# Performance work log

Hardware: AMD Instinct MI355X
Metric: run time of the kernel (lower is better)

## Reference

```python
import jax, jax.numpy as jnp
import numpy as np

B, N, NE, C = 1, 50000, 400000, 128
NTOK, NHEAD = 64, 4
HID = 256


def setup_inputs() -> dict:
    key = jax.random.key(0)
    ks = jax.random.split(key, 48)
    i = [0]
    def nx(shape, s=0.05):
        k = ks[i[0]]; i[0] += 1
        return jax.random.normal(k, shape, jnp.float32) * s
    inp = {}
    inp['V'] = nx((B, N, C), 1.0)
    inp['E'] = nx((B, NE, C), 1.0)
    kidx = ks[i[0]]; i[0] += 1
    inp['edges'] = jax.random.randint(kidx, (B, NE, 2), 0, N, dtype=jnp.int32)
    inp['F_space'] = jnp.zeros((B, N, 45), jnp.float32)
    # GNN f_edge: Linear(384->256), GELU, Linear(256->128), LayerNorm(128)
    inp['fe_w1'] = nx((HID, 3 * C)); inp['fe_b1'] = nx((HID,))
    inp['fe_w2'] = nx((C, HID));     inp['fe_b2'] = nx((C,))
    inp['fe_g'] = jnp.ones((C,));    inp['fe_be'] = jnp.zeros((C,))
    # GNN f_node: Linear(256->256), GELU, Linear(256->128), LayerNorm(128)
    inp['fn_w1'] = nx((HID, 2 * C)); inp['fn_b1'] = nx((HID,))
    inp['fn_w2'] = nx((C, HID));     inp['fn_b2'] = nx((C,))
    inp['fn_g'] = jnp.ones((C,));    inp['fn_be'] = jnp.zeros((C,))
    inp['ln1_g'] = jnp.ones((C,));   inp['ln1_b'] = jnp.zeros((C,))
    inp['ln2_g'] = jnp.ones((C,));   inp['ln2_b'] = jnp.zeros((C,))
    inp['lin_w'] = nx((C, C));       inp['lin_b'] = nx((C,))
    # AttentionBlock params
    inp['Qp'] = nx((NTOK, C), 1.0)
    inp['q1_w'] = nx((C, C)); inp['q1_b'] = nx((C,))
    inp['k1_w'] = nx((C, C)); inp['k1_b'] = nx((C,))
    inp['v1_w'] = nx((C, C)); inp['v1_b'] = nx((C,))
    inp['mha_in_w'] = nx((3 * C, C)); inp['mha_in_b'] = nx((3 * C,))
    inp['mha_out_w'] = nx((C, C));    inp['mha_out_b'] = nx((C,))
    inp['q2_w'] = nx((C, C)); inp['q2_b'] = nx((C,))
    inp['k2_w'] = nx((C, C)); inp['k2_b'] = nx((C,))
    inp['v2_w'] = nx((C, C)); inp['v2_b'] = nx((C,))
    # alphas (init 0 in the original; randomized here so gates are non-trivial)
    inp['a1'] = nx((1,), 0.5); inp['a2'] = nx((1,), 0.5)
    inp['a3'] = nx((1,), 0.5); inp['a4'] = nx((1,), 0.5)
    return inp


def _ln(x, g, b, eps=1e-5):
    m = jnp.mean(x, -1, keepdims=True)
    v = jnp.mean((x - m) ** 2, -1, keepdims=True)
    return (x - m) / jnp.sqrt(v + eps) * g + b


def _lin(x, w, b):
    return x @ w.T + b


def _gelu(x):
    return jax.nn.gelu(x, approximate=False)


def reference(V, E, edges, F_space, fe_w1, fe_b1, fe_w2, fe_b2, fe_g, fe_be,
              fn_w1, fn_b1, fn_w2, fn_b2, fn_g, fn_be, ln1_g, ln1_b, ln2_g, ln2_b,
              lin_w, lin_b, Qp, q1_w, q1_b, k1_w, k1_b, v1_w, v1_b,
              mha_in_w, mha_in_b, mha_out_w, mha_out_b, q2_w, q2_b, k2_w, k2_b,
              v2_w, v2_b, a1, a2, a3, a4):
    b, n, c = V.shape
    ne = edges.shape[1]
    # ---- GNN: gather -> edge MLP -> scatter_mean -> node MLP ----
    senders = jnp.take_along_axis(V, edges[..., 0:1], axis=1)    # [B,Ne,C]
    receivers = jnp.take_along_axis(V, edges[..., 1:2], axis=1)  # [B,Ne,C]
    edge_inpt = jnp.concatenate([senders, receivers, E], axis=-1)  # [B,Ne,3C]
    e_emb = _ln(_lin(_gelu(_lin(edge_inpt, fe_w1, fe_b1)), fe_w2, fe_b2), fe_g, fe_be)
    seg = (edges[..., 1] + jnp.arange(b, dtype=edges.dtype)[:, None] * n).reshape(-1)
    esum = jax.ops.segment_sum(e_emb.reshape(b * ne, c), seg, num_segments=b * n)
    cnt = jax.ops.segment_sum(jnp.ones((b * ne,), e_emb.dtype), seg, num_segments=b * n)
    edge_mean = (esum / jnp.maximum(cnt, 1.0)[:, None]).reshape(b, n, c)
    node_inpt = jnp.concatenate([V, edge_mean], axis=-1)
    v_emb = _ln(_lin(_gelu(_lin(node_inpt, fn_w1, fn_b1)), fn_w2, fn_b2), fn_g, fn_be)
    # ---- gated residuals (idx=0 < n_blocks=4) ----
    silu = jax.nn.silu
    Vr = V + silu(a1) * v_emb
    E_out = E + silu(a2) * e_emb
    # ---- dual cross-attention ----
    W0 = _ln(Vr, ln1_g, ln1_b)
    scale = c ** (-0.5)
    Q1 = _lin(jnp.broadcast_to(Qp, (b, NTOK, c)), q1_w, q1_b)
    K1 = _lin(W0, k1_w, k1_b)
    V1 = _lin(W0, v1_w, v1_b)
    attn1 = jax.nn.softmax(jnp.einsum('bmc,bnc->bmn', Q1, K1) * scale, axis=-1)
    W1 = attn1 @ V1  # [B,NTOK,C]
    # nn.MultiheadAttention(W1, W1, W1)
    h = c // NHEAD
    qkv = W1 @ mha_in_w.T + mha_in_b
    q, k, v = jnp.split(qkv, 3, axis=-1)
    sp = lambda t: t.reshape(b, NTOK, NHEAD, h).transpose(0, 2, 1, 3)
    q, k, v = sp(q), sp(k), sp(v)
    a = jax.nn.softmax(jnp.einsum('bhqd,bhkd->bhqk', q, k) * (h ** -0.5), axis=-1)
    o = jnp.einsum('bhqk,bhkd->bhqd', a, v).transpose(0, 2, 1, 3).reshape(b, NTOK, c)
    W2 = o @ mha_out_w.T + mha_out_b
    Q2 = _lin(W0, q2_w, q2_b)
    K2 = _lin(W2, k2_w, k2_b)
    V2 = _lin(W2, v2_w, v2_b)
    attn2 = jax.nn.softmax(jnp.einsum('bnc,bmc->bnm', Q2, K2) * scale, axis=-1)
    W3a = attn2 @ V2  # [B,N,C]
    W2r = Vr + silu(a3) * W3a
    W3 = W2r + silu(a4) * _lin(_ln(W2r, ln2_g, ln2_b), lin_w, lin_b)
    return (W3, E_out)
```

## Files before the change

### kernel.cpp

```cpp
#include <hip/hip_runtime.h>
#include <hip/hip_bf16.h>

#define NN 50000
#define NEDGE 400000
#define CDIM 128
#define NSP 50048

typedef short bf16x8 __attribute__((ext_vector_type(8)));
typedef short bf16x4 __attribute__((ext_vector_type(4)));
typedef float f32x4 __attribute__((ext_vector_type(4)));

__device__ __forceinline__ short f2b(float f) {
  union { float f; unsigned u; } a; a.f = f;
  unsigned u = a.u;
  u += 0x7fffu + ((u >> 16) & 1u);
  return (short)(u >> 16);
}
__device__ __forceinline__ float b2f(short s) {
  union { unsigned u; float f; } a; a.u = ((unsigned)(unsigned short)s) << 16;
  return a.f;
}
__device__ __forceinline__ float geluf(float x) {
  return 0.5f * x * (1.0f + erff(x * 0.7071067811865475f));
}
__device__ __forceinline__ f32x4 mfma16(bf16x8 a, bf16x8 b, f32x4 c) {
  return __builtin_amdgcn_mfma_f32_16x16x32_bf16(a, b, c, 0, 0, 0);
}

__global__ __launch_bounds__(256) void prep_kernel(
    const float* few1, const float* few2, const float* fnw1, const float* fnw2,
    const float* k1w, const float* v1w, const float* q2w,
    const float* k1b, const float* v1b, const float* q2b,
    const float* linw,
    short* wb1, short* wb2, short* wn1, short* wn2,
    short* wkvq, float* bkvq, short* wlin)
{
  int i = blockIdx.x * blockDim.x + threadIdx.x;
  int nthr = gridDim.x * blockDim.x;
  const float scale = 0.0883883476483184f;
  for (int idx = i; idx < 98304; idx += nthr) wb1[idx] = f2b(few1[idx]);
  for (int idx = i; idx < 32768; idx += nthr) wb2[idx] = f2b(few2[idx]);
  for (int idx = i; idx < 65536; idx += nthr) wn1[idx] = f2b(fnw1[idx]);
  for (int idx = i; idx < 32768; idx += nthr) wn2[idx] = f2b(fnw2[idx]);
  for (int idx = i; idx < 16384; idx += nthr) {
    wkvq[idx]         = f2b(k1w[idx]);
    wkvq[16384 + idx] = f2b(v1w[idx]);
    wkvq[32768 + idx] = f2b(q2w[idx] * scale);
    wlin[idx]         = f2b(linw[idx]);
  }
  for (int idx = i; idx < 128; idx += nthr) {
    bkvq[idx]       = k1b[idx];
    bkvq[128 + idx] = v1b[idx];
    bkvq[256 + idx] = q2b[idx] * scale;
  }
}

__global__ __launch_bounds__(256) void q1_kernel(
    const float* Qp, const float* q1w, const float* q1b, short* q1bf)
{
  int idx = blockIdx.x * 256 + threadIdx.x;
  int m = idx >> 7, n = idx & 127;
  const float scale = 0.0883883476483184f;
  float s = q1b[n];
  const float* qr = Qp + m * CDIM;
  const float* wr = q1w + n * CDIM;
  for (int k = 0; k < CDIM; k++) s += qr[k] * wr[k];
  q1bf[idx] = f2b(s * scale);
}

__global__ __launch_bounds__(256) void edge_kernel(
    const float* __restrict__ V, const float* __restrict__ E,
    const int* __restrict__ edges,
    const short* __restrict__ wb1, const float* __restrict__ fb1,
    const short* __restrict__ wb2, const float* __restrict__ fb2,
    const float* __restrict__ feg, const float* __restrict__ febe,
    const float* __restrict__ a2p,
    float* __restrict__ accn, float* __restrict__ cnt,
    float* __restrict__ outE)
{
  __shared__ short xs[64 * 392];
  __shared__ float redS[64][4], redQ[64][4];
  __shared__ int recvl[64];
  const int t = threadIdx.x;
  const int e0 = blockIdx.x * 64;
  if (t < 64) recvl[t] = edges[(e0 + t) * 2 + 1];
#pragma unroll
  for (int p = 0; p < 24; p++) {
    int fid = p * 256 + t;
    int row = fid / 96;
    int c = fid - row * 96;
    int seg = c >> 5;
    int c4 = c & 31;
    const float* src;
    if (seg == 0)      src = V + (size_t)edges[(e0 + row) * 2]     * CDIM + c4 * 4;
    else if (seg == 1) src = V + (size_t)edges[(e0 + row) * 2 + 1] * CDIM + c4 * 4;
    else               src = E + (size_t)(e0 + row) * CDIM + c4 * 4;
    f32x4 v = *(const f32x4*)src;
    bf16x4 bb; bb[0] = f2b(v[0]); bb[1] = f2b(v[1]); bb[2] = f2b(v[2]); bb[3] = f2b(v[3]);
    *(bf16x4*)(&xs[row * 392 + seg * 128 + c4 * 4]) = bb;
  }
  __syncthreads();
  const int lane = t & 63, wid = t >> 6;
  const int lr = lane & 15;
  const int g4 = (lane >> 4) * 4;
  const int lk = (lane >> 4) * 8;
  f32x4 acc1[4][4];
#pragma unroll
  for (int nt = 0; nt < 4; nt++) {
    float bv = fb1[wid * 64 + nt * 16 + lr];
#pragma unroll
    for (int mt = 0; mt < 4; mt++) acc1[mt][nt] = (f32x4){bv, bv, bv, bv};
  }
  for (int s = 0; s < 12; s++) {
    bf16x8 af[4];
#pragma unroll
    for (int mt = 0; mt < 4; mt++)
      af[mt] = *(const bf16x8*)(&xs[(mt * 16 + lr) * 392 + s * 32 + lk]);
#pragma unroll
    for (int nt = 0; nt < 4; nt++) {
      bf16x8 bf = *(const bf16x8*)(wb1 + (size_t)(wid * 64 + nt * 16 + lr) * 384 + s * 32 + lk);
#pragma unroll
      for (int mt = 0; mt < 4; mt++) acc1[mt][nt] = mfma16(af[mt], bf, acc1[mt][nt]);
    }
  }
  __syncthreads();
  short* hs = xs;
#pragma unroll
  for (int mt = 0; mt < 4; mt++)
#pragma unroll
    for (int nt = 0; nt < 4; nt++)
#pragma unroll
      for (int i = 0; i < 4; i++)
        hs[(mt * 16 + g4 + i) * 264 + wid * 64 + nt * 16 + lr] = f2b(geluf(acc1[mt][nt][i]));
  __syncthreads();
  f32x4 acc2[4][2];
#pragma unroll
  for (int nt = 0; nt < 2; nt++) {
    float bv = fb2[wid * 32 + nt * 16 + lr];
#pragma unroll
    for (int mt = 0; mt < 4; mt++) acc2[mt][nt] = (f32x4){bv, bv, bv, bv};
  }
  for (int s = 0; s < 8; s++) {
    bf16x8 af[4];
#pragma unroll
    for (int mt = 0; mt < 4; mt++)
      af[mt] = *(const bf16x8*)(&hs[(mt * 16 + lr) * 264 + s * 32 + lk]);
#pragma unroll
    for (int nt = 0; nt < 2; nt++) {
      bf16x8 bf = *(const bf16x8*)(wb2 + (size_t)(wid * 32 + nt * 16 + lr) * 256 + s * 32 + lk);
#pragma unroll
      for (int mt = 0; mt < 4; mt++) acc2[mt][nt] = mfma16(af[mt], bf, acc2[mt][nt]);
    }
  }
#pragma unroll
  for (int mt = 0; mt < 4; mt++)
#pragma unroll
    for (int i = 0; i < 4; i++) {
      float s1 = acc2[mt][0][i] + acc2[mt][1][i];
      float s2 = acc2[mt][0][i] * acc2[mt][0][i] + acc2[mt][1][i] * acc2[mt][1][i];
#pragma unroll
      for (int m = 1; m <= 8; m <<= 1) { s1 += __shfl_xor(s1, m); s2 += __shfl_xor(s2, m); }
      if (lr == 0) { redS[mt * 16 + g4 + i][wid] = s1; redQ[mt * 16 + g4 + i][wid] = s2; }
    }
  __syncthreads();
  float a2v = a2p[0];
  float sa2 = a2v / (1.0f + __expf(-a2v));
  float mean[4][4], rstd[4][4];
#pragma unroll
  for (int mt = 0; mt < 4; mt++)
#pragma unroll
    for (int i = 0; i < 4; i++) {
      int row = mt * 16 + g4 + i;
      float s1 = redS[row][0] + redS[row][1] + redS[row][2] + redS[row][3];
      float s2 = redQ[row][0] + redQ[row][1] + redQ[row][2] + redQ[row][3];
      float mn = s1 * (1.0f / 128.0f);
      float var = s2 * (1.0f / 128.0f) - mn * mn;
      mean[mt][i] = mn;
      rstd[mt][i] = rsqrtf(var + 1e-5f);
    }
#pragma unroll
  for (int nt = 0; nt < 2; nt++) {
    int col = wid * 32 + nt * 16 + lr;
    float gg = feg[col], bb = febe[col];
#pragma unroll
    for (int mt = 0; mt < 4; mt++)
#pragma unroll
      for (int i = 0; i < 4; i++) {
        int row = mt * 16 + g4 + i;
        float v = (acc2[mt][nt][i] - mean[mt][i]) * rstd[mt][i] * gg + bb;
        size_t ge = (size_t)(e0 + row) * CDIM + col;
        outE[ge] = E[ge] + sa2 * v;
        atomicAdd(&accn[(size_t)recvl[row] * CDIM + col], v);
      }
  }
  if (wid == 0 && lr == 0) {
#pragma unroll
    for (int mt = 0; mt < 4; mt++)
#pragma unroll
      for (int i = 0; i < 4; i++)
        atomicAdd(&cnt[recvl[mt * 16 + g4 + i]], 1.0f);
  }
}

__global__ __launch_bounds__(256) void node_kernel(
    const float* __restrict__ V, const float* __restrict__ accn, const float* __restrict__ cnt,
    const short* __restrict__ wn1, const float* __restrict__ fnb1,
    const short* __restrict__ wn2, const float* __restrict__ fnb2,
    const float* __restrict__ fng, const float* __restrict__ fnbe,
    const float* __restrict__ ln1g, const float* __restrict__ ln1b,
    const float* __restrict__ a1p,
    float* __restrict__ Vr, short* __restrict__ W0bf)
{
  __shared__ short xs[64 * 264];
  __shared__ float redS[64][4], redQ[64][4], redS2[64][4], redQ2[64][4];
  const int t = threadIdx.x;
  const int n0 = blockIdx.x * 64;
#pragma unroll
  for (int p = 0; p < 16; p++) {
    int fid = p * 256 + t;
    int row = fid >> 6;
    int c = fid & 63;
    int node = n0 + row; if (node >= NN) node = NN - 1;
    f32x4 v;
    if (c < 32) v = *(const f32x4*)(V + (size_t)node * CDIM + c * 4);
    else {
      v = *(const f32x4*)(accn + (size_t)node * CDIM + (c - 32) * 4);
      float ic = 1.0f / fmaxf(cnt[node], 1.0f);
      v[0] *= ic; v[1] *= ic; v[2] *= ic; v[3] *= ic;
    }
    bf16x4 bb; bb[0] = f2b(v[0]); bb[1] = f2b(v[1]); bb[2] = f2b(v[2]); bb[3] = f2b(v[3]);
    *(bf16x4*)(&xs[row * 264 + c * 4]) = bb;
  }
  __syncthreads();
  const int lane = t & 63, wid = t >> 6;
  const int lr = lane & 15;
  const int g4 = (lane >> 4) * 4;
  const int lk = (lane >> 4) * 8;
  f32x4 acc1[4][4];
#pragma unroll
  for (int nt = 0; nt < 4; nt++) {
    float bv = fnb1[wid * 64 + nt * 16 + lr];
#pragma unroll
    for (int mt = 0; mt < 4; mt++) acc1[mt][nt] = (f32x4){bv, bv, bv, bv};
  }
  for (int s = 0; s < 8; s++) {
    bf16x8 af[4];
#pragma unroll
    for (int mt = 0; mt < 4; mt++)
      af[mt] = *(const bf16x8*)(&xs[(mt * 16 + lr) * 264 + s * 32 + lk]);
#pragma unroll
    for (int nt = 0; nt < 4; nt++) {
      bf16x8 bf = *(const bf16x8*)(wn1 + (size_t)(wid * 64 + nt * 16 + lr) * 256 + s * 32 + lk);
#pragma unroll
      for (int mt = 0; mt < 4; mt++) acc1[mt][nt] = mfma16(af[mt], bf, acc1[mt][nt]);
    }
  }
  __syncthreads();
  short* hs = xs;
#pragma unroll
  for (int mt = 0; mt < 4; mt++)
#pragma unroll
    for (int nt = 0; nt < 4; nt++)
#pragma unroll
      for (int i = 0; i < 4; i++)
        hs[(mt * 16 + g4 + i) * 264 + wid * 64 + nt * 16 + lr] = f2b(geluf(acc1[mt][nt][i]));
  __syncthreads();
  f32x4 acc2[4][2];
#pragma unroll
  for (int nt = 0; nt < 2; nt++) {
    float bv = fnb2[wid * 32 + nt * 16 + lr];
#pragma unroll
    for (int mt = 0; mt < 4; mt++) acc2[mt][nt] = (f32x4){bv, bv, bv, bv};
  }
  for (int s = 0; s < 8; s++) {
    bf16x8 af[4];
#pragma unroll
    for (int mt = 0; mt < 4; mt++)
      af[mt] = *(const bf16x8*)(&hs[(mt * 16 + lr) * 264 + s * 32 + lk]);
#pragma unroll
    for (int nt = 0; nt < 2; nt++) {
      bf16x8 bf = *(const bf16x8*)(wn2 + (size_t)(wid * 32 + nt * 16 + lr) * 256 + s * 32 + lk);
#pragma unroll
      for (int mt = 0; mt < 4; mt++) acc2[mt][nt] = mfma16(af[mt], bf, acc2[mt][nt]);
    }
  }
#pragma unroll
  for (int mt = 0; mt < 4; mt++)
#pragma unroll
    for (int i = 0; i < 4; i++) {
      float s1 = acc2[mt][0][i] + acc2[mt][1][i];
      float s2 = acc2[mt][0][i] * acc2[mt][0][i] + acc2[mt][1][i] * acc2[mt][1][i];
#pragma unroll
      for (int m = 1; m <= 8; m <<= 1) { s1 += __shfl_xor(s1, m); s2 += __shfl_xor(s2, m); }
      if (lr == 0) { redS[mt * 16 + g4 + i][wid] = s1; redQ[mt * 16 + g4 + i][wid] = s2; }
    }
  __syncthreads();
  float a1v = a1p[0];
  float sa1 = a1v / (1.0f + __expf(-a1v));
  float mean[4][4], rstd[4][4];
#pragma unroll
  for (int mt = 0; mt < 4; mt++)
#pragma unroll
    for (int i = 0; i < 4; i++) {
      int row = mt * 16 + g4 + i;
      float s1 = redS[row][0] + redS[row][1] + redS[row][2] + redS[row][3];
      float s2 = redQ[row][0] + redQ[row][1] + redQ[row][2] + redQ[row][3];
      float mn = s1 * (1.0f / 128.0f);
      float var = s2 * (1.0f / 128.0f) - mn * mn;
      mean[mt][i] = mn; rstd[mt][i] = rsqrtf(var + 1e-5f);
    }
#pragma unroll
  for (int nt = 0; nt < 2; nt++) {
    int col = wid * 32 + nt * 16 + lr;
    float gg = fng[col], bb = fnbe[col];
#pragma unroll
    for (int mt = 0; mt < 4; mt++)
#pragma unroll
      for (int i = 0; i < 4; i++) {
        int row = mt * 16 + g4 + i;
        int node = n0 + row;
        int nc = node < NN ? node : NN - 1;
        float vemb = (acc2[mt][nt][i] - mean[mt][i]) * rstd[mt][i] * gg + bb;
        float vr = V[(size_t)nc * CDIM + col] + sa1 * vemb;
        acc2[mt][nt][i] = vr;
        if (node < NN) Vr[(size_t)node * CDIM + col] = vr;
      }
  }
#pragma unroll
  for (int mt = 0; mt < 4; mt++)
#pragma unroll
    for (int i = 0; i < 4; i++) {
      float s1 = acc2[mt][0][i] + acc2[mt][1][i];
      float s2 = acc2[mt][0][i] * acc2[mt][0][i] + acc2[mt][1][i] * acc2[mt][1][i];
#pragma unroll
      for (int m = 1; m <= 8; m <<= 1) { s1 += __shfl_xor(s1, m); s2 += __shfl_xor(s2, m); }
      if (lr == 0) { redS2[mt * 16 + g4 + i][wid] = s1; redQ2[mt * 16 + g4 + i][wid] = s2; }
    }
  __syncthreads();
#pragma unroll
  for (int mt = 0; mt < 4; mt++)
#pragma unroll
    for (int i = 0; i < 4; i++) {
      int row = mt * 16 + g4 + i;
      float s1 = redS2[row][0] + redS2[row][1] + redS2[row][2] + redS2[row][3];
      float s2 = redQ2[row][0] + redQ2[row][1] + redQ2[row][2] + redQ2[row][3];
      float mn = s1 * (1.0f / 128.0f);
      float var = s2 * (1.0f / 128.0f) - mn * mn;
      mean[mt][i] = mn; rstd[mt][i] = rsqrtf(var + 1e-5f);
    }
#pragma unroll
  for (int nt = 0; nt < 2; nt++) {
    int col = wid * 32 + nt * 16 + lr;
    float gg = ln1g[col], bb = ln1b[col];
#pragma unroll
    for (int mt = 0; mt < 4; mt++)
#pragma unroll
      for (int i = 0; i < 4; i++) {
        int row = mt * 16 + g4 + i;
        int node = n0 + row;
        if (node < NN)
          W0bf[(size_t)node * CDIM + col] =
              f2b((acc2[mt][nt][i] - mean[mt][i]) * rstd[mt][i] * gg + bb);
      }
  }
}

__global__ __launch_bounds__(256) void kvq_kernel(
    const short* __restrict__ W0bf, const short* __restrict__ wkvq,
    const float* __restrict__ bkvq,
    short* __restrict__ K1bf, short* __restrict__ V1bf, short* __restrict__ Q2bf)
{
  const int t = threadIdx.x, lane = t & 63, wid = t >> 6;
  const int n0 = blockIdx.x * 64;
  const int m0 = wid * 16, lr = lane & 15, lk = (lane >> 4) * 8;
  f32x4 acc[24];
#pragma unroll
  for (int tt = 0; tt < 24; tt++) {
    float bv = bkvq[tt * 16 + lr];
    acc[tt] = (f32x4){bv, bv, bv, bv};
  }
  int arow = n0 + m0 + lr; if (arow >= NN) arow = NN - 1;
  for (int s = 0; s < 4; s++) {
    bf16x8 a = *(const bf16x8*)(W0bf + (size_t)arow * CDIM + s * 32 + lk);
#pragma unroll
    for (int tt = 0; tt < 24; tt++) {
      bf16x8 b = *(const bf16x8*)(wkvq + (size_t)(tt * 16 + lr) * CDIM + s * 32 + lk);
      acc[tt] = mfma16(a, b, acc[tt]);
    }
  }
  const int r0 = m0 + (lane >> 4) * 4;
#pragma unroll
  for (int tt = 0; tt < 24; tt++) {
    int col = (tt & 7) * 16 + lr;
    short* dst = tt < 8 ? K1bf : (tt < 16 ? V1bf : Q2bf);
#pragma unroll
    for (int i = 0; i < 4; i++) {
      int node = n0 + r0 + i;
      if (node < NN) dst[(size_t)node * CDIM + col] = f2b(acc[tt][i]);
    }
  }
}

__global__ __launch_bounds__(256) void s_kernel(
    const short* __restrict__ q1bf, const short* __restrict__ K1bf, float* __restrict__ S)
{
  const int t = threadIdx.x, lane = t & 63, wid = t >> 6;
  const int nb = blockIdx.x * 256 + wid * 64;
  const int lr = lane & 15, lk = (lane >> 4) * 8;
  f32x4 acc[4][4];
#pragma unroll
  for (int mt = 0; mt < 4; mt++)
#pragma unroll
    for (int nt = 0; nt < 4; nt++) acc[mt][nt] = (f32x4){0.f, 0.f, 0.f, 0.f};
  for (int s = 0; s < 4; s++) {
    bf16x8 a[4], b[4];
#pragma unroll
    for (int mt = 0; mt < 4; mt++)
      a[mt] = *(const bf16x8*)(q1bf + (size_t)(mt * 16 + lr) * CDIM + s * 32 + lk);
#pragma unroll
    for (int nt = 0; nt < 4; nt++) {
      int n = nb + nt * 16 + lr; if (n >= NN) n = NN - 1;
      b[nt] = *(const bf16x8*)(K1bf + (size_t)n * CDIM + s * 32 + lk);
    }
#pragma unroll
    for (int mt = 0; mt < 4; mt++)
#pragma unroll
      for (int nt = 0; nt < 4; nt++) acc[mt][nt] = mfma16(a[mt], b[nt], acc[mt][nt]);
  }
  const int g4 = (lane >> 4) * 4;
#pragma unroll
  for (int mt = 0; mt < 4; mt++)
#pragma unroll
    for (int nt = 0; nt < 4; nt++)
#pragma unroll
      for (int i = 0; i < 4; i++) {
        int q = mt * 16 + g4 + i;
        int n = nb + nt * 16 + lr;
        if (n < NN) S[(size_t)q * NSP + n] = acc[mt][nt][i];
      }
}

__global__ __launch_bounds__(256) void softmax_kernel(float* __restrict__ S)
{
  __shared__ float red[8];
  float* row = S + (size_t)blockIdx.x * NSP;
  const int t = threadIdx.x;
  float m = -1e30f;
  for (int n = t; n < NN; n += 256) m = fmaxf(m, row[n]);
  for (int sh = 1; sh < 64; sh <<= 1) m = fmaxf(m, __shfl_xor(m, sh));
  if ((t & 63) == 0) red[t >> 6] = m;
  __syncthreads();
  m = fmaxf(fmaxf(red[0], red[1]), fmaxf(red[2], red[3]));
  float sum = 0.f;
  for (int n = t; n < NN; n += 256) sum += __expf(row[n] - m);
  for (int sh = 1; sh < 64; sh <<= 1) sum += __shfl_xor(sum, sh);
  if ((t & 63) == 0) red[4 + (t >> 6)] = sum;
  __syncthreads();
  sum = red[4] + red[5] + red[6] + red[7];
  float inv = 1.0f / sum;
  for (int n = t; n < NN; n += 256) row[n] = __expf(row[n] - m) * inv;
}

__global__ __launch_bounds__(256) void w1_kernel(
    const float* __restrict__ S, const short* __restrict__ V1bf, float* __restrict__ W1)
{
  const int t = threadIdx.x;
  const int c4 = t & 31;
  const int qb = t >> 5;
  const int chunk = (NN + 127) / 128;
  int ns = blockIdx.x * chunk;
  int nend = ns + chunk; if (nend > NN) nend = NN;
  f32x4 acc[8];
#pragma unroll
  for (int p = 0; p < 8; p++) acc[p] = (f32x4){0.f, 0.f, 0.f, 0.f};
  for (int n = ns; n < nend; n++) {
    bf16x4 vb = *(const bf16x4*)(V1bf + (size_t)n * CDIM + c4 * 4);
    f32x4 v; v[0] = b2f(vb[0]); v[1] = b2f(vb[1]); v[2] = b2f(vb[2]); v[3] = b2f(vb[3]);
#pragma unroll
    for (int p = 0; p < 8; p++) {
      float pv = S[(size_t)(p * 8 + qb) * NSP + n];
      acc[p][0] += pv * v[0]; acc[p][1] += pv * v[1];
      acc[p][2] += pv * v[2]; acc[p][3] += pv * v[3];
    }
  }
#pragma unroll
  for (int p = 0; p < 8; p++)
#pragma unroll
    for (int j = 0; j < 4; j++)
      atomicAdd(&W1[(size_t)(p * 8 + qb) * CDIM + c4 * 4 + j], acc[p][j]);
}

__global__ __launch_bounds__(256) void qkv_kernel(
    const float* __restrict__ W1, const float* __restrict__ inw,
    const float* __restrict__ inb, float* __restrict__ qkv)
{
  int idx = blockIdx.x * 256 + threadIdx.x;
  int m = idx / 384, n = idx - m * 384;
  float s = inb[n];
  const float* wr = inw + (size_t)n * CDIM;
  const float* xr = W1 + (size_t)m * CDIM;
  for (int k = 0; k < CDIM; k++) s += xr[k] * wr[k];
  qkv[idx] = s;
}

__global__ __launch_bounds__(256) void heads_kernel(
    const float* __restrict__ qkv, float* __restrict__ o)
{
  __shared__ float q[64][33], k[64][33], v[64][33], sc[64][65];
  const int h = blockIdx.x, t = threadIdx.x;
#pragma unroll
  for (int p = 0; p < 8; p++) {
    int idx = p * 256 + t;
    int i = idx >> 5, d = idx & 31;
    q[i][d] = qkv[i * 384 + h * 32 + d];
    k[i][d] = qkv[i * 384 + 128 + h * 32 + d];
    v[i][d] = qkv[i * 384 + 256 + h * 32 + d];
  }
  __syncthreads();
  const float rs = 0.1767766952966369f;
#pragma unroll
  for (int p = 0; p < 16; p++) {
    int idx = p * 256 + t;
    int i = idx >> 6, j = idx & 63;
    float s = 0.f;
    for (int d = 0; d < 32; d++) s += q[i][d] * k[j][d];
    sc[i][j] = s * rs;
  }
  __syncthreads();
  if (t < 64) {
    float m = -1e30f;
    for (int j = 0; j < 64; j++) m = fmaxf(m, sc[t][j]);
    float sum = 0.f;
    for (int j = 0; j < 64; j++) { float e = __expf(sc[t][j] - m); sc[t][j] = e; sum += e; }
    float inv = 1.0f / sum;
    for (int j = 0; j < 64; j++) sc[t][j] *= inv;
  }
  __syncthreads();
#pragma unroll
  for (int p = 0; p < 8; p++) {
    int idx = p * 256 + t;
    int i = idx >> 5, d = idx & 31;
    float s = 0.f;
    for (int j = 0; j < 64; j++) s += sc[i][j] * v[j][d];
    o[i * CDIM + h * 32 + d] = s;
  }
}

__global__ __launch_bounds__(256) void w2_kernel(
    const float* __restrict__ o, const float* __restrict__ ow,
    const float* __restrict__ ob, float* __restrict__ W2)
{
  int idx = blockIdx.x * 256 + threadIdx.x;
  int m = idx >> 7, n = idx & 127;
  float s = ob[n];
  for (int kk = 0; kk < CDIM; kk++) s += o[m * CDIM + kk] * ow[n * CDIM + kk];
  W2[idx] = s;
}

__global__ __launch_bounds__(256) void kv2_kernel(
    const float* __restrict__ W2,
    const float* __restrict__ k2w, const float* __restrict__ k2b,
    const float* __restrict__ v2w, const float* __restrict__ v2b,
    short* __restrict__ k2bf, short* __restrict__ v2tbf)
{
  int idx = blockIdx.x * 256 + threadIdx.x;
  int which = idx >> 13;
  int r = (idx >> 7) & 63, n = idx & 127;
  const float* w = which ? v2w : k2w;
  float s = which ? v2b[n] : k2b[n];
  for (int kk = 0; kk < CDIM; kk++) s += W2[r * CDIM + kk] * w[n * CDIM + kk];
  if (which) v2tbf[n * 64 + r] = f2b(s);
  else       k2bf[r * CDIM + n] = f2b(s);
}

__global__ __launch_bounds__(256) void g_kernel(
    const short* __restrict__ Q2bf, const short* __restrict__ k2bf,
    const short* __restrict__ v2tbf,
    const short* __restrict__ wlin, const float* __restrict__ linb,
    const float* __restrict__ ln2g, const float* __restrict__ ln2b,
    const float* __restrict__ Vr, const float* __restrict__ a3p,
    const float* __restrict__ a4p, float* __restrict__ outW)
{
  __shared__ short p_lds[64 * 72];
  __shared__ short t_lds[64 * 136];
  const int t = threadIdx.x, lane = t & 63, wid = t >> 6;
  const int n0 = blockIdx.x * 64;
  const int m0 = wid * 16, lr = lane & 15, lk = (lane >> 4) * 8;
  const int r0 = m0 + (lane >> 4) * 4;
  int arow = n0 + m0 + lr; if (arow >= NN) arow = NN - 1;
  f32x4 sacc[4];
#pragma unroll
  for (int nt = 0; nt < 4; nt++) sacc[nt] = (f32x4){0.f, 0.f, 0.f, 0.f};
  for (int s = 0; s < 4; s++) {
    bf16x8 a = *(const bf16x8*)(Q2bf + (size_t)arow * CDIM + s * 32 + lk);
#pragma unroll
    for (int nt = 0; nt < 4; nt++) {
      bf16x8 b = *(const bf16x8*)(k2bf + (size_t)(nt * 16 + lr) * CDIM + s * 32 + lk);
      sacc[nt] = mfma16(a, b, sacc[nt]);
    }
  }
  float mx[4], sum[4];
#pragma unroll
  for (int i = 0; i < 4; i++) {
    float m = fmaxf(fmaxf(sacc[0][i], sacc[1][i]), fmaxf(sacc[2][i], sacc[3][i]));
#pragma unroll
    for (int sh = 1; sh <= 8; sh <<= 1) m = fmaxf(m, __shfl_xor(m, sh));
    mx[i] = m; sum[i] = 0.f;
  }
#pragma unroll
  for (int nt = 0; nt < 4; nt++)
#pragma unroll
    for (int i = 0; i < 4; i++) {
      float e = __expf(sacc[nt][i] - mx[i]);
      sacc[nt][i] = e; sum[i] += e;
    }
#pragma unroll
  for (int i = 0; i < 4; i++) {
#pragma unroll
    for (int sh = 1; sh <= 8; sh <<= 1) sum[i] += __shfl_xor(sum[i], sh);
    sum[i] = 1.0f / sum[i];
  }
#pragma unroll
  for (int nt = 0; nt < 4; nt++)
#pragma unroll
    for (int i = 0; i < 4; i++)
      p_lds[(r0 + i) * 72 + nt * 16 + lr] = f2b(sacc[nt][i] * sum[i]);
  __syncthreads();
  f32x4 oacc[8];
#pragma unroll
  for (int tt = 0; tt < 8; tt++) oacc[tt] = (f32x4){0.f, 0.f, 0.f, 0.f};
  for (int s = 0; s < 2; s++) {
    bf16x8 a = *(const bf16x8*)(&p_lds[(m0 + lr) * 72 + s * 32 + lk]);
#pragma unroll
    for (int tt = 0; tt < 8; tt++) {
      bf16x8 b = *(const bf16x8*)(v2tbf + (size_t)(tt * 16 + lr) * 64 + s * 32 + lk);
      oacc[tt] = mfma16(a, b, oacc[tt]);
    }
  }
  float a3v = a3p[0]; float sa3 = a3v / (1.0f + __expf(-a3v));
  float a4v = a4p[0]; float sa4 = a4v / (1.0f + __expf(-a4v));
  float w2r[8][4];
  float sum2[4] = {0.f, 0.f, 0.f, 0.f}, sq2[4] = {0.f, 0.f, 0.f, 0.f};
#pragma unroll
  for (int tt = 0; tt < 8; tt++) {
    int col = tt * 16 + lr;
#pragma unroll
    for (int i = 0; i < 4; i++) {
      int node = n0 + r0 + i;
      int nc = node < NN ? node : NN - 1;
      float vr = Vr[(size_t)nc * CDIM + col];
      float w = vr + sa3 * oacc[tt][i];
      w2r[tt][i] = w;
      sum2[i] += w; sq2[i] += w * w;
    }
  }
#pragma unroll
  for (int sh = 1; sh <= 8; sh <<= 1)
#pragma unroll
    for (int i = 0; i < 4; i++) {
      sum2[i] += __shfl_xor(sum2[i], sh);
      sq2[i] += __shfl_xor(sq2[i], sh);
    }
  float mean[4], rstd[4];
#pragma unroll
  for (int i = 0; i < 4; i++) {
    mean[i] = sum2[i] * (1.0f / 128.0f);
    float var = sq2[i] * (1.0f / 128.0f) - mean[i] * mean[i];
    rstd[i] = rsqrtf(var + 1e-5f);
  }
#pragma unroll
  for (int tt = 0; tt < 8; tt++) {
    int col = tt * 16 + lr;
    float gg = ln2g[col], bb = ln2b[col];
#pragma unroll
    for (int i = 0; i < 4; i++)
      t_lds[(r0 + i) * 136 + col] = f2b((w2r[tt][i] - mean[i]) * rstd[i] * gg + bb);
  }
  __syncthreads();
  f32x4 yacc[8];
#pragma unroll
  for (int tt = 0; tt < 8; tt++) {
    float bv = linb[tt * 16 + lr];
    yacc[tt] = (f32x4){bv, bv, bv, bv};
  }
  for (int s = 0; s < 4; s++) {
    bf16x8 a = *(const bf16x8*)(&t_lds[(m0 + lr) * 136 + s * 32 + lk]);
#pragma unroll
    for (int tt = 0; tt < 8; tt++) {
      bf16x8 b = *(const bf16x8*)(wlin + (size_t)(tt * 16 + lr) * CDIM + s * 32 + lk);
      yacc[tt] = mfma16(a, b, yacc[tt]);
    }
  }
#pragma unroll
  for (int tt = 0; tt < 8; tt++) {
    int col = tt * 16 + lr;
#pragma unroll
    for (int i = 0; i < 4; i++) {
      int node = n0 + r0 + i;
      if (node < NN) outW[(size_t)node * CDIM + col] = w2r[tt][i] + sa4 * yacc[tt][i];
    }
  }
}

extern "C" void kernel_launch(void* const* d_in, const int* in_sizes, int n_in,
                              void* d_out, int out_size, void* d_ws, size_t ws_size,
                              hipStream_t stream) {
  const float* V      = (const float*)d_in[0];
  const float* E      = (const float*)d_in[1];
  const int*   edges  = (const int*)d_in[2];
  const float* fe_w1  = (const float*)d_in[4];
  const float* fe_b1  = (const float*)d_in[5];
  const float* fe_w2  = (const float*)d_in[6];
  const float* fe_b2  = (const float*)d_in[7];
  const float* fe_g   = (const float*)d_in[8];
  const float* fe_be  = (const float*)d_in[9];
  const float* fn_w1  = (const float*)d_in[10];
  const float* fn_b1  = (const float*)d_in[11];
  const float* fn_w2  = (const float*)d_in[12];
  const float* fn_b2  = (const float*)d_in[13];
  const float* fn_g   = (const float*)d_in[14];
  const float* fn_be  = (const float*)d_in[15];
  const float* ln1_g  = (const float*)d_in[16];
  const float* ln1_b  = (const float*)d_in[17];
  const float* ln2_g  = (const float*)d_in[18];
  const float* ln2_b  = (const float*)d_in[19];
  const float* lin_w  = (const float*)d_in[20];
  const float* lin_b  = (const float*)d_in[21];
  const float* Qp     = (const float*)d_in[22];
  const float* q1_w   = (const float*)d_in[23];
  const float* q1_b   = (const float*)d_in[24];
  const float* k1_w   = (const float*)d_in[25];
  const float* k1_b   = (const float*)d_in[26];
  const float* v1_w   = (const float*)d_in[27];
  const float* v1_b   = (const float*)d_in[28];
  const float* mha_in_w  = (const float*)d_in[29];
  const float* mha_in_b  = (const float*)d_in[30];
  const float* mha_out_w = (const float*)d_in[31];
  const float* mha_out_b = (const float*)d_in[32];
  const float* q2_w   = (const float*)d_in[33];
  const float* q2_b   = (const float*)d_in[34];
  const float* k2_w   = (const float*)d_in[35];
  const float* k2_b   = (const float*)d_in[36];
  const float* v2_w   = (const float*)d_in[37];
  const float* v2_b   = (const float*)d_in[38];
  const float* a1 = (const float*)d_in[39];
  const float* a2 = (const float*)d_in[40];
  const float* a3 = (const float*)d_in[41];
  const float* a4 = (const float*)d_in[42];

  char* ws = (char*)d_ws;
  constexpr size_t OFF_WB1  = 0;
  constexpr size_t OFF_WB2  = OFF_WB1 + 98304u * 2;
  constexpr size_t OFF_WN1  = OFF_WB2 + 32768u * 2;
  constexpr size_t OFF_WN2  = OFF_WN1 + 65536u * 2;
  constexpr size_t OFF_WKVQ = OFF_WN2 + 32768u * 2;
  constexpr size_t OFF_BKVQ = OFF_WKVQ + 49152u * 2;
  constexpr size_t OFF_WLIN = OFF_BKVQ + 2048;
  constexpr size_t OFF_Q1   = OFF_WLIN + 16384u * 2;
  constexpr size_t OFF_K2B  = OFF_Q1 + 8192u * 2;
  constexpr size_t OFF_V2T  = OFF_K2B + 8192u * 2;
  constexpr size_t OFF_W1   = OFF_V2T + 8192u * 2;
  constexpr size_t OFF_QKV  = OFF_W1 + 8192u * 4;
  constexpr size_t OFF_O    = OFF_QKV + 24576u * 4;
  constexpr size_t OFF_W2   = OFF_O + 8192u * 4;
  constexpr size_t OFF_ACC  = (OFF_W2 + 8192u * 4 + 255) & ~(size_t)255;
  constexpr size_t OFF_CNT  = OFF_ACC + (size_t)NN * CDIM * 4;
  constexpr size_t OFF_VR   = OFF_CNT + ((NN * 4 + 255) & ~(size_t)255);
  constexpr size_t OFF_W0   = OFF_VR + (size_t)NN * CDIM * 4;
  constexpr size_t OFF_K1   = OFF_W0 + (size_t)NN * CDIM * 2;
  constexpr size_t OFF_V1   = OFF_K1 + (size_t)NN * CDIM * 2;
  constexpr size_t OFF_Q2   = OFF_V1 + (size_t)NN * CDIM * 2;

  short* wb1   = (short*)(ws + OFF_WB1);
  short* wb2   = (short*)(ws + OFF_WB2);
  short* wn1   = (short*)(ws + OFF_WN1);
  short* wn2   = (short*)(ws + OFF_WN2);
  short* wkvq  = (short*)(ws + OFF_WKVQ);
  float* bkvq  = (float*)(ws + OFF_BKVQ);
  short* wlin  = (short*)(ws + OFF_WLIN);
  short* q1bf  = (short*)(ws + OFF_Q1);
  short* k2bf  = (short*)(ws + OFF_K2B);
  short* v2tbf = (short*)(ws + OFF_V2T);
  float* W1    = (float*)(ws + OFF_W1);
  float* qkv   = (float*)(ws + OFF_QKV);
  float* o     = (float*)(ws + OFF_O);
  float* W2    = (float*)(ws + OFF_W2);
  float* accn  = (float*)(ws + OFF_ACC);
  float* S     = (float*)(ws + OFF_ACC);
  float* cnt   = (float*)(ws + OFF_CNT);
  float* Vr    = (float*)(ws + OFF_VR);
  short* W0bf  = (short*)(ws + OFF_W0);
  short* K1bf  = (short*)(ws + OFF_K1);
  short* V1bf  = (short*)(ws + OFF_V1);
  short* Q2bf  = (short*)(ws + OFF_Q2);

  float* outW = (float*)d_out;
  float* outE = outW + (size_t)NN * CDIM;

  hipMemsetAsync(accn, 0, (size_t)NN * CDIM * 4, stream);
  hipMemsetAsync(cnt, 0, (size_t)NN * 4, stream);
  hipMemsetAsync(W1, 0, 8192u * 4, stream);

  prep_kernel<<<256, 256, 0, stream>>>(fe_w1, fe_w2, fn_w1, fn_w2,
                                       k1_w, v1_w, q2_w, k1_b, v1_b, q2_b,
                                       lin_w, wb1, wb2, wn1, wn2, wkvq, bkvq, wlin);
  q1_kernel<<<32, 256, 0, stream>>>(Qp, q1_w, q1_b, q1bf);
  edge_kernel<<<NEDGE / 64, 256, 0, stream>>>(V, E, edges, wb1, fe_b1, wb2, fe_b2,
                                              fe_g, fe_be, a2, accn, cnt, outE);
  node_kernel<<<(NN + 63) / 64, 256, 0, stream>>>(V, accn, cnt, wn1, fn_b1, wn2, fn_b2,
                                                  fn_g, fn_be, ln1_g, ln1_b, a1, Vr, W0bf);
  kvq_kernel<<<(NN + 63) / 64, 256, 0, stream>>>(W0bf, wkvq, bkvq, K1bf, V1bf, Q2bf);
  s_kernel<<<(NN + 255) / 256, 256, 0, stream>>>(q1bf, K1bf, S);
  softmax_kernel<<<64, 256, 0, stream>>>(S);
  w1_kernel<<<128, 256, 0, stream>>>(S, V1bf, W1);
  qkv_kernel<<<96, 256, 0, stream>>>(W1, mha_in_w, mha_in_b, qkv);
  heads_kernel<<<4, 256, 0, stream>>>(qkv, o);
  w2_kernel<<<32, 256, 0, stream>>>(o, mha_out_w, mha_out_b, W2);
  kv2_kernel<<<64, 256, 0, stream>>>(W2, k2_w, k2_b, v2_w, v2_b, k2bf, v2tbf);
  g_kernel<<<(NN + 63) / 64, 256, 0, stream>>>(Q2bf, k2bf, v2tbf, wlin, lin_b,
                                               ln2_g, ln2_b, Vr, a3, a4, outW);
}
```

Baseline: 1.989 ms.

## Restructure edge MLP to per-wave 32-edge tiles with pre-converted bf16 V

Adds a pass that converts V to bf16 once, so edge gathers read half the bytes and skip per-edge conversion. The edge kernel is rewritten so each 64-thread wave owns 32 edges. Weights become the MFMA A operand read directly from global, and gathered rows feed registers without a shared staging buffer. The hidden layer goes through a swizzled per-wave LDS tile, LayerNorm is reduced with shuffles instead of block barriers, and outE is written with coalesced vector stores. This trades more weight reads per edge and higher register pressure (32 accumulators) for fewer block-wide syncs and less gather traffic. The bf16 V reuses the Vr buffer, which node_kernel overwrites later.

```diff
diff --git a/kernel.cpp b/kernel.cpp
--- a/kernel.cpp
+++ b/kernel.cpp
@@ -25,6 +25,12 @@
 }
 __device__ __forceinline__ f32x4 mfma16(bf16x8 a, bf16x8 b, f32x4 c) {
   return __builtin_amdgcn_mfma_f32_16x16x32_bf16(a, b, c, 0, 0, 0);
+}
+__device__ __forceinline__ bf16x8 pk8(f32x4 a, f32x4 b) {
+  bf16x8 r;
+  r[0] = f2b(a[0]); r[1] = f2b(a[1]); r[2] = f2b(a[2]); r[3] = f2b(a[3]);
+  r[4] = f2b(b[0]); r[5] = f2b(b[1]); r[6] = f2b(b[2]); r[7] = f2b(b[3]);
+  return r;
 }
 
 __global__ __launch_bounds__(256) void prep_kernel(
@@ -55,6 +61,18 @@
   }
 }
 
+__global__ __launch_bounds__(256) void conv_v_kernel(const float* __restrict__ V,
+                                                     short* __restrict__ Vbf)
+{
+  int i = blockIdx.x * 256 + threadIdx.x;
+  int nthr = gridDim.x * 256;
+  for (int idx = i; idx < NN * CDIM / 4; idx += nthr) {
+    f32x4 v = *(const f32x4*)(V + (size_t)idx * 4);
+    bf16x4 b; b[0] = f2b(v[0]); b[1] = f2b(v[1]); b[2] = f2b(v[2]); b[3] = f2b(v[3]);
+    *(bf16x4*)(Vbf + (size_t)idx * 4) = b;
+  }
+}
+
 __global__ __launch_bounds__(256) void q1_kernel(
     const float* Qp, const float* q1w, const float* q1b, short* q1bf)
 {
@@ -68,8 +86,8 @@
   q1bf[idx] = f2b(s * scale);
 }
 
-__global__ __launch_bounds__(256) void edge_kernel(
-    const float* __restrict__ V, const float* __restrict__ E,
+__global__ __launch_bounds__(128) void edge2_kernel(
+    const short* __restrict__ Vbf, const float* __restrict__ E,
     const int* __restrict__ edges,
     const short* __restrict__ wb1, const float* __restrict__ fb1,
     const short* __restrict__ wb2, const float* __restrict__ fb2,
@@ -78,127 +96,139 @@
     float* __restrict__ accn, float* __restrict__ cnt,
     float* __restrict__ outE)
 {
-  __shared__ short xs[64 * 392];
-  __shared__ float redS[64][4], redQ[64][4];
-  __shared__ int recvl[64];
-  const int t = threadIdx.x;
-  const int e0 = blockIdx.x * 64;
-  if (t < 64) recvl[t] = edges[(e0 + t) * 2 + 1];
-#pragma unroll
-  for (int p = 0; p < 24; p++) {
-    int fid = p * 256 + t;
-    int row = fid / 96;
-    int c = fid - row * 96;
-    int seg = c >> 5;
-    int c4 = c & 31;
-    const float* src;
-    if (seg == 0)      src = V + (size_t)edges[(e0 + row) * 2]     * CDIM + c4 * 4;
-    else if (seg == 1) src = V + (size_t)edges[(e0 + row) * 2 + 1] * CDIM + c4 * 4;
-    else               src = E + (size_t)(e0 + row) * CDIM + c4 * 4;
-    f32x4 v = *(const f32x4*)src;
-    bf16x4 bb; bb[0] = f2b(v[0]); bb[1] = f2b(v[1]); bb[2] = f2b(v[2]); bb[3] = f2b(v[3]);
-    *(bf16x4*)(&xs[row * 392 + seg * 128 + c4 * 4]) = bb;
-  }
-  __syncthreads();
-  const int lane = t & 63, wid = t >> 6;
-  const int lr = lane & 15;
-  const int g4 = (lane >> 4) * 4;
-  const int lk = (lane >> 4) * 8;
-  f32x4 acc1[4][4];
-#pragma unroll
-  for (int nt = 0; nt < 4; nt++) {
-    float bv = fb1[wid * 64 + nt * 16 + lr];
-#pragma unroll
-    for (int mt = 0; mt < 4; mt++) acc1[mt][nt] = (f32x4){bv, bv, bv, bv};
-  }
-  for (int s = 0; s < 12; s++) {
-    bf16x8 af[4];
-#pragma unroll
-    for (int mt = 0; mt < 4; mt++)
-      af[mt] = *(const bf16x8*)(&xs[(mt * 16 + lr) * 392 + s * 32 + lk]);
-#pragma unroll
-    for (int nt = 0; nt < 4; nt++) {
-      bf16x8 bf = *(const bf16x8*)(wb1 + (size_t)(wid * 64 + nt * 16 + lr) * 384 + s * 32 + lk);
-#pragma unroll
-      for (int mt = 0; mt < 4; mt++) acc1[mt][nt] = mfma16(af[mt], bf, acc1[mt][nt]);
-    }
-  }
-  __syncthreads();
-  short* hs = xs;
-#pragma unroll
-  for (int mt = 0; mt < 4; mt++)
-#pragma unroll
-    for (int nt = 0; nt < 4; nt++)
-#pragma unroll
-      for (int i = 0; i < 4; i++)
-        hs[(mt * 16 + g4 + i) * 264 + wid * 64 + nt * 16 + lr] = f2b(geluf(acc1[mt][nt][i]));
-  __syncthreads();
-  f32x4 acc2[4][2];
-#pragma unroll
-  for (int nt = 0; nt < 2; nt++) {
-    float bv = fb2[wid * 32 + nt * 16 + lr];
-#pragma unroll
-    for (int mt = 0; mt < 4; mt++) acc2[mt][nt] = (f32x4){bv, bv, bv, bv};
-  }
-  for (int s = 0; s < 8; s++) {
-    bf16x8 af[4];
-#pragma unroll
-    for (int mt = 0; mt < 4; mt++)
-      af[mt] = *(const bf16x8*)(&hs[(mt * 16 + lr) * 264 + s * 32 + lk]);
-#pragma unroll
-    for (int nt = 0; nt < 2; nt++) {
-      bf16x8 bf = *(const bf16x8*)(wb2 + (size_t)(wid * 32 + nt * 16 + lr) * 256 + s * 32 + lk);
-#pragma unroll
-      for (int mt = 0; mt < 4; mt++) acc2[mt][nt] = mfma16(af[mt], bf, acc2[mt][nt]);
-    }
-  }
-#pragma unroll
-  for (int mt = 0; mt < 4; mt++)
-#pragma unroll
-    for (int i = 0; i < 4; i++) {
-      float s1 = acc2[mt][0][i] + acc2[mt][1][i];
-      float s2 = acc2[mt][0][i] * acc2[mt][0][i] + acc2[mt][1][i] * acc2[mt][1][i];
-#pragma unroll
-      for (int m = 1; m <= 8; m <<= 1) { s1 += __shfl_xor(s1, m); s2 += __shfl_xor(s2, m); }
-      if (lr == 0) { redS[mt * 16 + g4 + i][wid] = s1; redQ[mt * 16 + g4 + i][wid] = s2; }
-    }
-  __syncthreads();
+  __shared__ __align__(16) char hsm[2][16384];
+  const int t = threadIdx.x, lane = t & 63, wid = t >> 6;
+  const int lr = lane & 15, g = lane >> 4;
+  const int ebase = blockIdx.x * 64 + wid * 32;
+  const int eA = ebase + lr;
+  const int eB = ebase + 16 + lr;
+  const int sA = edges[eA * 2],     rA = edges[eA * 2 + 1];
+  const int sB = edges[eB * 2],     rB = edges[eB * 2 + 1];
+  char* hp = hsm[wid];
+  const int swz = (lr & 7) << 4;
+
+  f32x4 acc1[16][2];
+#pragma unroll
+  for (int nt = 0; nt < 16; nt++) {
+    f32x4 b4 = *(const f32x4*)(fb1 + nt * 16 + g * 4);
+    acc1[nt][0] = b4; acc1[nt][1] = b4;
+  }
+  const char* pVA = (const char*)Vbf + (size_t)sA * 256;
+  const char* pVB = (const char*)Vbf + (size_t)sB * 256;
+  const char* pRA = (const char*)Vbf + (size_t)rA * 256;
+  const char* pRB = (const char*)Vbf + (size_t)rB * 256;
+#pragma unroll
+  for (int s = 0; s < 4; s++) {
+    bf16x8 x0 = *(const bf16x8*)(pVA + s * 64 + g * 16);
+    bf16x8 x1 = *(const bf16x8*)(pVB + s * 64 + g * 16);
+#pragma unroll
+    for (int nt = 0; nt < 16; nt++) {
+      bf16x8 wf = *(const bf16x8*)(wb1 + (size_t)(nt * 16 + lr) * 384 + s * 32 + g * 8);
+      acc1[nt][0] = mfma16(wf, x0, acc1[nt][0]);
+      acc1[nt][1] = mfma16(wf, x1, acc1[nt][1]);
+    }
+  }
+#pragma unroll
+  for (int s = 0; s < 4; s++) {
+    bf16x8 x0 = *(const bf16x8*)(pRA + s * 64 + g * 16);
+    bf16x8 x1 = *(const bf16x8*)(pRB + s * 64 + g * 16);
+#pragma unroll
+    for (int nt = 0; nt < 16; nt++) {
+      bf16x8 wf = *(const bf16x8*)(wb1 + (size_t)(nt * 16 + lr) * 384 + 128 + s * 32 + g * 8);
+      acc1[nt][0] = mfma16(wf, x0, acc1[nt][0]);
+      acc1[nt][1] = mfma16(wf, x1, acc1[nt][1]);
+    }
+  }
+#pragma unroll
+  for (int s = 0; s < 4; s++) {
+    f32x4 a0 = *(const f32x4*)(E + (size_t)eA * 128 + s * 32 + g * 8);
+    f32x4 a1 = *(const f32x4*)(E + (size_t)eA * 128 + s * 32 + g * 8 + 4);
+    f32x4 b0 = *(const f32x4*)(E + (size_t)eB * 128 + s * 32 + g * 8);
+    f32x4 b1 = *(const f32x4*)(E + (size_t)eB * 128 + s * 32 + g * 8 + 4);
+    bf16x8 x0 = pk8(a0, a1);
+    bf16x8 x1 = pk8(b0, b1);
+#pragma unroll
+    for (int nt = 0; nt < 16; nt++) {
+      bf16x8 wf = *(const bf16x8*)(wb1 + (size_t)(nt * 16 + lr) * 384 + 256 + s * 32 + g * 8);
+      acc1[nt][0] = mfma16(wf, x0, acc1[nt][0]);
+      acc1[nt][1] = mfma16(wf, x1, acc1[nt][1]);
+    }
+  }
+#pragma unroll
+  for (int mt = 0; mt < 2; mt++) {
+    int m = mt * 16 + lr;
+#pragma unroll
+    for (int nt = 0; nt < 16; nt++) {
+      f32x4 v = acc1[nt][mt];
+      unsigned lo = (unsigned)(unsigned short)f2b(geluf(v[0])) |
+                    ((unsigned)(unsigned short)f2b(geluf(v[1])) << 16);
+      unsigned hi = (unsigned)(unsigned short)f2b(geluf(v[2])) |
+                    ((unsigned)(unsigned short)f2b(geluf(v[3])) << 16);
+      uint2 d; d.x = lo; d.y = hi;
+      *(uint2*)(hp + ((m * 512 + nt * 32 + g * 8) ^ swz)) = d;
+    }
+  }
+  f32x4 acc2[8][2];
+#pragma unroll
+  for (int nt = 0; nt < 8; nt++) {
+    f32x4 b4 = *(const f32x4*)(fb2 + nt * 16 + g * 4);
+    acc2[nt][0] = b4; acc2[nt][1] = b4;
+  }
+#pragma unroll
+  for (int s2 = 0; s2 < 8; s2++) {
+    bf16x8 h0 = *(const bf16x8*)(hp + ((lr * 512 + s2 * 64 + g * 16) ^ swz));
+    bf16x8 h1 = *(const bf16x8*)(hp + (((16 + lr) * 512 + s2 * 64 + g * 16) ^ swz));
+#pragma unroll
+    for (int nt = 0; nt < 8; nt++) {
+      bf16x8 wf = *(const bf16x8*)(wb2 + (size_t)(nt * 16 + lr) * 256 + s2 * 32 + g * 8);
+      acc2[nt][0] = mfma16(wf, h0, acc2[nt][0]);
+      acc2[nt][1] = mfma16(wf, h1, acc2[nt][1]);
+    }
+  }
   float a2v = a2p[0];
   float sa2 = a2v / (1.0f + __expf(-a2v));
-  float mean[4][4], rstd[4][4];
-#pragma unroll
-  for (int mt = 0; mt < 4; mt++)
-#pragma unroll
-    for (int i = 0; i < 4; i++) {
-      int row = mt * 16 + g4 + i;
-      float s1 = redS[row][0] + redS[row][1] + redS[row][2] + redS[row][3];
-      float s2 = redQ[row][0] + redQ[row][1] + redQ[row][2] + redQ[row][3];
-      float mn = s1 * (1.0f / 128.0f);
-      float var = s2 * (1.0f / 128.0f) - mn * mn;
-      mean[mt][i] = mn;
-      rstd[mt][i] = rsqrtf(var + 1e-5f);
-    }
-#pragma unroll
-  for (int nt = 0; nt < 2; nt++) {
-    int col = wid * 32 + nt * 16 + lr;
-    float gg = feg[col], bb = febe[col];
-#pragma unroll
-    for (int mt = 0; mt < 4; mt++)
+#pragma unroll
+  for (int mt = 0; mt < 2; mt++) {
+    float s1 = 0.f, sq = 0.f;
+#pragma unroll
+    for (int nt = 0; nt < 8; nt++)
 #pragma unroll
       for (int i = 0; i < 4; i++) {
-        int row = mt * 16 + g4 + i;
-        float v = (acc2[mt][nt][i] - mean[mt][i]) * rstd[mt][i] * gg + bb;
-        size_t ge = (size_t)(e0 + row) * CDIM + col;
-        outE[ge] = E[ge] + sa2 * v;
-        atomicAdd(&accn[(size_t)recvl[row] * CDIM + col], v);
+        float v = acc2[nt][mt][i];
+        s1 += v; sq += v * v;
       }
-  }
-  if (wid == 0 && lr == 0) {
-#pragma unroll
-    for (int mt = 0; mt < 4; mt++)
-#pragma unroll
-      for (int i = 0; i < 4; i++)
-        atomicAdd(&cnt[recvl[mt * 16 + g4 + i]], 1.0f);
+    s1 += __shfl_xor(s1, 16); sq += __shfl_xor(sq, 16);
+    s1 += __shfl_xor(s1, 32); sq += __shfl_xor(sq, 32);
+    float mn = s1 * (1.0f / 128.0f);
+    float var = sq * (1.0f / 128.0f) - mn * mn;
+    float rstd = rsqrtf(var + 1e-5f);
+    int recv = mt ? rB : rA;
+#pragma unroll
+    for (int nt = 0; nt < 8; nt++) {
+      f32x4 g4 = *(const f32x4*)(feg + nt * 16 + g * 4);
+      f32x4 be4 = *(const f32x4*)(febe + nt * 16 + g * 4);
+      f32x4 v = acc2[nt][mt];
+#pragma unroll
+      for (int i = 0; i < 4; i++) {
+        float e = (v[i] - mn) * rstd * g4[i] + be4[i];
+        v[i] = e;
+        atomicAdd(accn + (size_t)recv * 128 + nt * 16 + g * 4 + i, e);
+      }
+      *(f32x4*)(hp + (((mt * 16 + lr) * 512 + nt * 64 + g * 16) ^ swz)) = v;
+    }
+  }
+  if (lane < 32) atomicAdd(cnt + edges[(ebase + lane) * 2 + 1], 1.0f);
+#pragma unroll
+  for (int r2 = 0; r2 < 16; r2++) {
+    int row = r2 * 2 + (lane >> 5);
+    int cb = (lane & 31) * 16;
+    f32x4 em = *(const f32x4*)(hp + ((row * 512 + cb) ^ ((row & 7) << 4)));
+    size_t gb = (size_t)(ebase + row) * 128 + (lane & 31) * 4;
+    f32x4 ev = *(const f32x4*)(E + gb);
+    f32x4 o;
+    o[0] = ev[0] + sa2 * em[0]; o[1] = ev[1] + sa2 * em[1];
+    o[2] = ev[2] + sa2 * em[2]; o[3] = ev[3] + sa2 * em[3];
+    *(f32x4*)(outE + gb) = o;
   }
 }
 
@@ -789,6 +819,7 @@
   float* S     = (float*)(ws + OFF_ACC);
   float* cnt   = (float*)(ws + OFF_CNT);
   float* Vr    = (float*)(ws + OFF_VR);
+  short* Vbf   = (short*)(ws + OFF_VR);
   short* W0bf  = (short*)(ws + OFF_W0);
   short* K1bf  = (short*)(ws + OFF_K1);
   short* V1bf  = (short*)(ws + OFF_V1);
@@ -804,9 +835,10 @@
   prep_kernel<<<256, 256, 0, stream>>>(fe_w1, fe_w2, fn_w1, fn_w2,
                                        k1_w, v1_w, q2_w, k1_b, v1_b, q2_b,
                                        lin_w, wb1, wb2, wn1, wn2, wkvq, bkvq, wlin);
+  conv_v_kernel<<<1600, 256, 0, stream>>>(V, Vbf);
   q1_kernel<<<32, 256, 0, stream>>>(Qp, q1_w, q1_b, q1bf);
-  edge_kernel<<<NEDGE / 64, 256, 0, stream>>>(V, E, edges, wb1, fe_b1, wb2, fe_b2,
-                                              fe_g, fe_be, a2, accn, cnt, outE);
+  edge2_kernel<<<NEDGE / 64, 128, 0, stream>>>(Vbf, E, edges, wb1, fe_b1, wb2, fe_b2,
+                                               fe_g, fe_be, a2, accn, cnt, outE);
   node_kernel<<<(NN + 63) / 64, 256, 0, stream>>>(V, accn, cnt, wn1, fn_b1, wn2, fn_b2,
                                                   fn_g, fn_be, ln1_g, ln1_b, a1, Vr, W0bf);
   kvq_kernel<<<(NN + 63) / 64, 256, 0, stream>>>(W0bf, wkvq, bkvq, K1bf, V1bf, Q2bf);
```

Result: slower. 2.280 ms (+14.6%).
